# Performance work log

Hardware: AMD Instinct MI355X
Metric: run time of the kernel (lower is better)

Reference implementation:

```python
import jax, jax.numpy as jnp
import numpy as np

B, T, C = 4, 2048, 1024
H = 16
HD = C // H


def setup_inputs() -> dict:
    key = jax.random.key(0)
    k1, k2, k3 = jax.random.split(key, 3)
    x = jax.random.normal(k1, (B, T, C), dtype=jnp.float32)
    w_qkv = jax.random.normal(k2, (C, 3 * C), dtype=jnp.float32) * (C ** -0.5)
    w_proj = jax.random.normal(k3, (C, C), dtype=jnp.float32) * (C ** -0.5)
    b_proj = jnp.zeros((C,), dtype=jnp.float32)
    return {"x": x, "w_qkv": w_qkv, "w_proj": w_proj, "b_proj": b_proj}


def reference(x, w_qkv, w_proj, b_proj):
    Bd, Td, Cd = x.shape
    scale = HD ** -0.5
    qkv = x @ w_qkv  # [B,T,3C]
    q, k, v = jnp.split(qkv, 3, axis=-1)
    # [B,H,T,HD]
    q = q.reshape(Bd, Td, H, HD).transpose(0, 2, 1, 3)
    k = k.reshape(Bd, Td, H, HD).transpose(0, 2, 1, 3)
    v = v.reshape(Bd, Td, H, HD).transpose(0, 2, 1, 3)
    att = jnp.einsum('bhqd,bhkd->bhqk', q, k) * scale
    causal = jnp.triu(jnp.ones((Td, Td), dtype=bool), k=1)
    att = jnp.where(causal, -jnp.inf, att)
    att = jax.nn.softmax(att, axis=-1)
    y = jnp.einsum('bhqk,bhkd->bhqd', att, v)
    y = y.transpose(0, 2, 1, 3).reshape(Bd, Td, Cd)
    return y @ w_proj + b_proj
```

## Files before the change

kernel.cpp:

```cpp
#include <hip/hip_runtime.h>

typedef unsigned short u16;
typedef __attribute__((ext_vector_type(8))) short short8;
typedef __attribute__((ext_vector_type(4))) float floatx4;
typedef __attribute__((ext_vector_type(4))) unsigned short ushort4v;

#define B_ 4
#define T_ 2048
#define C_ 1024
#define H_ 16
#define HD_ 64

static __device__ __forceinline__ u16 f2bf(float f) {
  union { float f; unsigned int i; } c; c.f = f;
  unsigned int u = c.i;
  return (u16)((u + 0x7FFFu + ((u >> 16) & 1u)) >> 16);
}

static __device__ __forceinline__ void gload16(const u16* g, u16* l) {
  __builtin_amdgcn_global_load_lds(
      (const __attribute__((address_space(1))) unsigned int*)(g),
      (__attribute__((address_space(3))) unsigned int*)(l), 16, 0, 0);
}

__global__ __launch_bounds__(256) void prep_k(const float* __restrict__ x,
                                              const float* __restrict__ w_qkv,
                                              const float* __restrict__ w_proj,
                                              u16* __restrict__ xbf,
                                              u16* __restrict__ wqkvT,
                                              u16* __restrict__ wprojT) {
  const int bid = blockIdx.x;
  if (bid < 8192) {
    const int i = bid * 256 + threadIdx.x;
    const float4 f = ((const float4*)x)[i];
    ushort4v o;
    o.x = f2bf(f.x); o.y = f2bf(f.y); o.z = f2bf(f.z); o.w = f2bf(f.w);
    *(ushort4v*)(xbf + (size_t)i * 4) = o;
    return;
  }
  __shared__ u16 tile[32][33];
  const float* in;
  u16* out;
  int R, Cc, tb;
  if (bid < 11264) {
    in = w_qkv; out = wqkvT; R = C_; Cc = 3 * C_; tb = bid - 8192;
  } else {
    in = w_proj; out = wprojT; R = C_; Cc = C_; tb = bid - 11264;
  }
  const int tpr = Cc / 32;
  const int bx = (tb % tpr) * 32;
  const int by = (tb / tpr) * 32;
  const int tx = threadIdx.x & 31;
  const int ty = threadIdx.x >> 5;
  #pragma unroll
  for (int i = ty; i < 32; i += 8)
    tile[i][tx] = f2bf(in[(size_t)(by + i) * Cc + bx + tx]);
  __syncthreads();
  #pragma unroll
  for (int i = ty; i < 32; i += 8)
    out[(size_t)(bx + i) * R + by + tx] = tile[tx][i];
}

__global__ __launch_bounds__(256) void vtrans_k(const u16* __restrict__ qkv,
                                                u16* __restrict__ vt) {
  __shared__ u16 tile[64][74];
  const int tt = blockIdx.x;
  const int bh = blockIdx.y;
  const int b = bh >> 4, h = bh & 15;
  const int tid = threadIdx.x;
  const u16* src = qkv + ((size_t)b * T_ + tt * 64) * (3 * C_) + 2 * C_ + h * HD_;
  #pragma unroll
  for (int ss = tid; ss < 512; ss += 256) {
    const int row = ss >> 3, c8 = (ss & 7) * 8;
    *(short8*)(&tile[row][c8]) = *(const short8*)(src + (size_t)row * (3 * C_) + c8);
  }
  __syncthreads();
  u16* dst = vt + (size_t)bh * HD_ * T_ + tt * 64;
  #pragma unroll
  for (int ss = tid; ss < 512; ss += 256) {
    const int tc = (ss & 7) * 8, d = ss >> 3;
    short8 o;
    #pragma unroll
    for (int j = 0; j < 8; j++) o[j] = (short)tile[tc + j][d];
    *(short8*)(dst + (size_t)d * T_ + tc) = o;
  }
}

template <int MODE>
__global__ __launch_bounds__(256) void gemm_bt(const u16* __restrict__ A,
                                               const u16* __restrict__ Bt,
                                               u16* __restrict__ outb,
                                               float* __restrict__ outf,
                                               const float* __restrict__ bias,
                                               int M, int N, int K) {
  __shared__ __align__(16) u16 As[2][128 * 32];
  __shared__ __align__(16) u16 Bs[2][128 * 32];
  const int tN = blockIdx.x * 128;
  const int tM = blockIdx.y * 128;
  const int tid = threadIdx.x;
  const int wave = tid >> 6;
  const int lane = tid & 63;
  const int lr = lane & 15;
  const int quad = lane >> 4;
  const int wm = (wave >> 1) * 64;
  const int wn = (wave & 1) * 64;

  const int srow = lane >> 2;
  const int skofs = ((lane & 3) ^ ((lane >> 3) & 3)) * 8;

  const floatx4 zf = {0.f, 0.f, 0.f, 0.f};
  floatx4 acc[4][4];
  #pragma unroll
  for (int i = 0; i < 4; i++)
    #pragma unroll
    for (int j = 0; j < 4; j++) acc[i][j] = zf;

  const int csw = (lr >> 1) & 3;

  for (int k0 = 0; k0 < K; k0 += 64) {
    __syncthreads();
    #pragma unroll
    for (int half = 0; half < 2; half++) {
      const int kk = k0 + half * 32;
      #pragma unroll
      for (int j = 0; j < 2; j++) {
        const int seg = wave * 2 + j;
        const int row = seg * 16 + srow;
        gload16(A + (size_t)(tM + row) * K + kk + skofs, &As[half][seg * 512]);
        gload16(Bt + (size_t)(tN + row) * K + kk + skofs, &Bs[half][seg * 512]);
      }
    }
    __syncthreads();

    #pragma unroll
    for (int half = 0; half < 2; half++) {
      short8 af[4], bfr[4];
      #pragma unroll
      for (int mt = 0; mt < 4; mt++)
        af[mt] = *(const short8*)(&As[half][(wm + mt * 16 + lr) * 32 + ((quad ^ csw) * 8)]);
      #pragma unroll
      for (int nt = 0; nt < 4; nt++)
        bfr[nt] = *(const short8*)(&Bs[half][(wn + nt * 16 + lr) * 32 + ((quad ^ csw) * 8)]);
      #pragma unroll
      for (int mt = 0; mt < 4; mt++)
        #pragma unroll
        for (int nt = 0; nt < 4; nt++)
          acc[mt][nt] = __builtin_amdgcn_mfma_f32_16x16x32_bf16(af[mt], bfr[nt],
                                                                acc[mt][nt], 0, 0, 0);
    }
  }

  #pragma unroll
  for (int mt = 0; mt < 4; mt++) {
    const int m0 = tM + wm + mt * 16 + quad * 4;
    #pragma unroll
    for (int nt = 0; nt < 4; nt++) {
      const int n = tN + wn + nt * 16 + lr;
      #pragma unroll
      for (int r = 0; r < 4; r++) {
        const float v = acc[mt][nt][r];
        const size_t m = (size_t)(m0 + r);
        if (MODE == 2) outf[m * N + n] = v + bias[n];
        else           outb[m * N + n] = f2bf(v);
      }
    }
  }
}

__global__ __launch_bounds__(256, 4) void attn_k(const u16* __restrict__ qkv,
                                                 const u16* __restrict__ vt,
                                                 u16* __restrict__ y) {
  __shared__ __align__(16) u16 Ks[64 * 64];
  __shared__ __align__(16) u16 Vs[64 * 64];
  __shared__ __align__(16) u16 PsA[4][16 * 72];
  __shared__ __align__(16) u16 PsB[4][16 * 72];
  const int qp = blockIdx.x;
  const int bh = blockIdx.y;
  const int b = bh >> 4, h = bh & 15;
  const int tid = threadIdx.x;
  const int wave = tid >> 6;
  const int lane = tid & 63;
  const int lr = lane & 15;
  const int quad = lane >> 4;
  const int qtA = qp, qtB = 31 - qp;

  const int srow = lane >> 3;
  const int skofs = ((lane & 7) ^ ((lane >> 3) & 7)) * 8;
  const int gsw = lr & 7;

  const size_t RS = 3 * C_;
  const u16* qcol = qkv + (size_t)b * T_ * RS + h * HD_;
  const u16* kcol = qcol + C_;

  const size_t qrA = (size_t)(qtA * 64 + wave * 16 + lr) * RS;
  const size_t qrB = (size_t)(qtB * 64 + wave * 16 + lr) * RS;
  const short8 aq0A = *(const short8*)(qcol + qrA + quad * 8);
  const short8 aq1A = *(const short8*)(qcol + qrA + 32 + quad * 8);
  const short8 aq0B = *(const short8*)(qcol + qrB + quad * 8);
  const short8 aq1B = *(const short8*)(qcol + qrB + 32 + quad * 8);

  const floatx4 zf = {0.f, 0.f, 0.f, 0.f};
  const float C1 = 0.125f * 1.44269504f;
  const float C2 = -16.0f * 1.44269504f;

  floatx4 accA[4], accB[4];
  #pragma unroll
  for (int i = 0; i < 4; i++) { accA[i] = zf; accB[i] = zf; }
  float psumA[4] = {0.f, 0.f, 0.f, 0.f}, psumB[4] = {0.f, 0.f, 0.f, 0.f};

  for (int kt = 0; kt <= qtB; kt++) {
    const bool doA = (kt <= qtA);
    const bool diagA = (kt == qtA), diagB = (kt == qtB);
    __syncthreads();
    #pragma unroll
    for (int j = 0; j < 2; j++) {
      const int seg = wave * 2 + j;
      const int row = seg * 8 + srow;
      gload16(kcol + (size_t)(kt * 64 + row) * RS + skofs, &Ks[seg * 512]);
      gload16(vt + ((size_t)bh * HD_ + row) * T_ + kt * 64 + skofs, &Vs[seg * 512]);
    }
    __syncthreads();

    #pragma unroll
    for (int nt = 0; nt < 4; nt++) {
      const short8 bk0 =
          *(const short8*)(&Ks[(nt * 16 + lr) * 64 + ((quad ^ gsw) * 8)]);
      const short8 bk1 =
          *(const short8*)(&Ks[(nt * 16 + lr) * 64 + (((quad + 4) ^ gsw) * 8)]);
      {
        floatx4 s = __builtin_amdgcn_mfma_f32_16x16x32_bf16(
            aq1B, bk1,
            __builtin_amdgcn_mfma_f32_16x16x32_bf16(aq0B, bk0, zf, 0, 0, 0),
            0, 0, 0);
        #pragma unroll
        for (int r = 0; r < 4; r++) {
          float pe = __builtin_amdgcn_exp2f(fmaf(s[r], C1, C2));
          if (diagB && (nt * 16 + lr > wave * 16 + quad * 4 + r)) pe = 0.f;
          psumB[r] += pe;
          union { float f; unsigned int i; } cc; cc.f = pe;
          PsB[wave][(quad * 4 + r) * 72 + nt * 16 + lr] = (u16)(cc.i >> 16);
        }
      }
      if (doA) {
        floatx4 s = __builtin_amdgcn_mfma_f32_16x16x32_bf16(
            aq1A, bk1,
            __builtin_amdgcn_mfma_f32_16x16x32_bf16(aq0A, bk0, zf, 0, 0, 0),
            0, 0, 0);
        #pragma unroll
        for (int r = 0; r < 4; r++) {
          float pe = __builtin_amdgcn_exp2f(fmaf(s[r], C1, C2));
          if (diagA && (nt * 16 + lr > wave * 16 + quad * 4 + r)) pe = 0.f;
          psumA[r] += pe;
          union { float f; unsigned int i; } cc; cc.f = pe;
          PsA[wave][(quad * 4 + r) * 72 + nt * 16 + lr] = (u16)(cc.i >> 16);
        }
      }
    }
    const short8 apB0 = *(const short8*)(&PsB[wave][lr * 72 + quad * 8]);
    const short8 apB1 = *(const short8*)(&PsB[wave][lr * 72 + 32 + quad * 8]);
    short8 apA0, apA1;
    if (doA) {
      apA0 = *(const short8*)(&PsA[wave][lr * 72 + quad * 8]);
      apA1 = *(const short8*)(&PsA[wave][lr * 72 + 32 + quad * 8]);
    }
    #pragma unroll
    for (int dt = 0; dt < 4; dt++) {
      const short8 bv0 =
          *(const short8*)(&Vs[(dt * 16 + lr) * 64 + ((quad ^ gsw) * 8)]);
      const short8 bv1 =
          *(const short8*)(&Vs[(dt * 16 + lr) * 64 + (((quad + 4) ^ gsw) * 8)]);
      accB[dt] = __builtin_amdgcn_mfma_f32_16x16x32_bf16(apB0, bv0, accB[dt], 0, 0, 0);
      accB[dt] = __builtin_amdgcn_mfma_f32_16x16x32_bf16(apB1, bv1, accB[dt], 0, 0, 0);
      if (doA) {
        accA[dt] = __builtin_amdgcn_mfma_f32_16x16x32_bf16(apA0, bv0, accA[dt], 0, 0, 0);
        accA[dt] = __builtin_amdgcn_mfma_f32_16x16x32_bf16(apA1, bv1, accA[dt], 0, 0, 0);
      }
    }
  }

  #pragma unroll
  for (int ph = 0; ph < 2; ph++) {
    const int qt = ph ? qtB : qtA;
    const floatx4* acc = ph ? accB : accA;
    const float* ps = ph ? psumB : psumA;
    const int rowg0 = qt * 64 + wave * 16 + quad * 4;
    #pragma unroll
    for (int r = 0; r < 4; r++) {
      float s = ps[r];
      #pragma unroll
      for (int off = 1; off < 16; off <<= 1) s += __shfl_xor(s, off, 64);
      const float inv = 1.f / s;
      const int t = rowg0 + r;
      #pragma unroll
      for (int dt = 0; dt < 4; dt++) {
        const int d = dt * 16 + lr;
        y[((size_t)(b * T_ + t)) * C_ + h * HD_ + d] = f2bf(acc[dt][r] * inv);
      }
    }
  }
}

extern "C" void kernel_launch(void* const* d_in, const int* in_sizes, int n_in,
                              void* d_out, int out_size, void* d_ws, size_t ws_size,
                              hipStream_t stream) {
  const float* x      = (const float*)d_in[0];
  const float* w_qkv  = (const float*)d_in[1];
  const float* w_proj = (const float*)d_in[2];
  const float* b_proj = (const float*)d_in[3];
  float* out = (float*)d_out;

  u16* ws = (u16*)d_ws;
  const size_t SZ = (size_t)B_ * T_ * C_;
  u16* xbf    = ws;
  u16* wqkvT  = xbf + SZ;
  u16* wprojT = wqkvT + (size_t)3 * C_ * C_;
  u16* qkvw   = wprojT + (size_t)C_ * C_;
  u16* vtw    = qkvw + 3 * SZ;
  u16* yw     = xbf;

  prep_k<<<12288, 256, 0, stream>>>(x, w_qkv, w_proj, xbf, wqkvT, wprojT);
  gemm_bt<1><<<dim3(3 * C_ / 128, B_ * T_ / 128), 256, 0, stream>>>(
      xbf, wqkvT, qkvw, nullptr, nullptr, B_ * T_, 3 * C_, C_);
  vtrans_k<<<dim3(T_ / 64, B_ * H_), 256, 0, stream>>>(qkvw, vtw);
  attn_k<<<dim3(16, B_ * H_), 256, 0, stream>>>(qkvw, vtw, yw);
  gemm_bt<2><<<dim3(C_ / 128, B_ * T_ / 128), 256, 0, stream>>>(
      yw, wprojT, nullptr, out, b_proj, B_ * T_, C_, C_);
}
```

Measured before the change: 266.6 us.

## Compute transposed scores so P stays in registers, dropping LDS round-trip

The score MFMA now computes S^T (K as the A operand, Q as B), so each lane holds exp'd probabilities already laid out as the B operand of the PV MFMA. This removes the per-wave P shared-memory buffers and their writes and reads. V fragments are gathered with split 4-element LDS reads to match the new k-ordering. The output is written as vectorized 4-element stores, and the row-sum reduction shrinks to two shuffles. The grid is flattened to 1D with a remapped block index, presumably to change how blocks are scheduled across heads. The changes add register pressure and 8-byte LDS reads in place of 16-byte ones.

```diff
diff --git a/kernel.cpp b/kernel.cpp
--- a/kernel.cpp
+++ b/kernel.cpp
@@ -2,6 +2,7 @@
 
 typedef unsigned short u16;
 typedef __attribute__((ext_vector_type(8))) short short8;
+typedef __attribute__((ext_vector_type(4))) short short4v;
 typedef __attribute__((ext_vector_type(4))) float floatx4;
 typedef __attribute__((ext_vector_type(4))) unsigned short ushort4v;
 
@@ -15,6 +16,10 @@
   union { float f; unsigned int i; } c; c.f = f;
   unsigned int u = c.i;
   return (u16)((u + 0x7FFFu + ((u >> 16) & 1u)) >> 16);
+}
+static __device__ __forceinline__ u16 truncbf(float f) {
+  union { float f; unsigned int i; } c; c.f = f;
+  return (u16)(c.i >> 16);
 }
 
 static __device__ __forceinline__ void gload16(const u16* g, u16* l) {
@@ -172,10 +177,10 @@
                                                  u16* __restrict__ y) {
   __shared__ __align__(16) u16 Ks[64 * 64];
   __shared__ __align__(16) u16 Vs[64 * 64];
-  __shared__ __align__(16) u16 PsA[4][16 * 72];
-  __shared__ __align__(16) u16 PsB[4][16 * 72];
-  const int qp = blockIdx.x;
-  const int bh = blockIdx.y;
+  const int bid = blockIdx.x;
+  const int s = bid >> 3;
+  const int qp = s >> 3;
+  const int bh = ((s & 7) << 3) | (bid & 7);
   const int b = bh >> 4, h = bh & 15;
   const int tid = threadIdx.x;
   const int wave = tid >> 6;
@@ -206,7 +211,7 @@
   floatx4 accA[4], accB[4];
   #pragma unroll
   for (int i = 0; i < 4; i++) { accA[i] = zf; accB[i] = zf; }
-  float psumA[4] = {0.f, 0.f, 0.f, 0.f}, psumB[4] = {0.f, 0.f, 0.f, 0.f};
+  float psumA = 0.f, psumB = 0.f;
 
   for (int kt = 0; kt <= qtB; kt++) {
     const bool doA = (kt <= qtA);
@@ -221,6 +226,7 @@
     }
     __syncthreads();
 
+    float peA[4][4], peB[4][4];
     #pragma unroll
     for (int nt = 0; nt < 4; nt++) {
       const short8 bk0 =
@@ -228,52 +234,57 @@
       const short8 bk1 =
           *(const short8*)(&Ks[(nt * 16 + lr) * 64 + (((quad + 4) ^ gsw) * 8)]);
       {
-        floatx4 s = __builtin_amdgcn_mfma_f32_16x16x32_bf16(
-            aq1B, bk1,
-            __builtin_amdgcn_mfma_f32_16x16x32_bf16(aq0B, bk0, zf, 0, 0, 0),
+        floatx4 st = __builtin_amdgcn_mfma_f32_16x16x32_bf16(
+            bk1, aq1B,
+            __builtin_amdgcn_mfma_f32_16x16x32_bf16(bk0, aq0B, zf, 0, 0, 0),
             0, 0, 0);
         #pragma unroll
         for (int r = 0; r < 4; r++) {
-          float pe = __builtin_amdgcn_exp2f(fmaf(s[r], C1, C2));
-          if (diagB && (nt * 16 + lr > wave * 16 + quad * 4 + r)) pe = 0.f;
-          psumB[r] += pe;
-          union { float f; unsigned int i; } cc; cc.f = pe;
-          PsB[wave][(quad * 4 + r) * 72 + nt * 16 + lr] = (u16)(cc.i >> 16);
+          float pe = __builtin_amdgcn_exp2f(fmaf(st[r], C1, C2));
+          if (diagB && (nt * 16 + quad * 4 + r > wave * 16 + lr)) pe = 0.f;
+          peB[nt][r] = pe;
+          psumB += pe;
         }
       }
       if (doA) {
-        floatx4 s = __builtin_amdgcn_mfma_f32_16x16x32_bf16(
-            aq1A, bk1,
-            __builtin_amdgcn_mfma_f32_16x16x32_bf16(aq0A, bk0, zf, 0, 0, 0),
+        floatx4 st = __builtin_amdgcn_mfma_f32_16x16x32_bf16(
+            bk1, aq1A,
+            __builtin_amdgcn_mfma_f32_16x16x32_bf16(bk0, aq0A, zf, 0, 0, 0),
             0, 0, 0);
         #pragma unroll
         for (int r = 0; r < 4; r++) {
-          float pe = __builtin_amdgcn_exp2f(fmaf(s[r], C1, C2));
-          if (diagA && (nt * 16 + lr > wave * 16 + quad * 4 + r)) pe = 0.f;
-          psumA[r] += pe;
-          union { float f; unsigned int i; } cc; cc.f = pe;
-          PsA[wave][(quad * 4 + r) * 72 + nt * 16 + lr] = (u16)(cc.i >> 16);
+          float pe = __builtin_amdgcn_exp2f(fmaf(st[r], C1, C2));
+          if (diagA && (nt * 16 + quad * 4 + r > wave * 16 + lr)) pe = 0.f;
+          peA[nt][r] = pe;
+          psumA += pe;
         }
       }
     }
-    const short8 apB0 = *(const short8*)(&PsB[wave][lr * 72 + quad * 8]);
-    const short8 apB1 = *(const short8*)(&PsB[wave][lr * 72 + 32 + quad * 8]);
-    short8 apA0, apA1;
-    if (doA) {
-      apA0 = *(const short8*)(&PsA[wave][lr * 72 + quad * 8]);
-      apA1 = *(const short8*)(&PsA[wave][lr * 72 + 32 + quad * 8]);
-    }
-    #pragma unroll
-    for (int dt = 0; dt < 4; dt++) {
-      const short8 bv0 =
-          *(const short8*)(&Vs[(dt * 16 + lr) * 64 + ((quad ^ gsw) * 8)]);
-      const short8 bv1 =
-          *(const short8*)(&Vs[(dt * 16 + lr) * 64 + (((quad + 4) ^ gsw) * 8)]);
-      accB[dt] = __builtin_amdgcn_mfma_f32_16x16x32_bf16(apB0, bv0, accB[dt], 0, 0, 0);
-      accB[dt] = __builtin_amdgcn_mfma_f32_16x16x32_bf16(apB1, bv1, accB[dt], 0, 0, 0);
-      if (doA) {
-        accA[dt] = __builtin_amdgcn_mfma_f32_16x16x32_bf16(apA0, bv0, accA[dt], 0, 0, 0);
-        accA[dt] = __builtin_amdgcn_mfma_f32_16x16x32_bf16(apA1, bv1, accA[dt], 0, 0, 0);
+
+    short8 pB[2], pA[2];
+    #pragma unroll
+    for (int h2 = 0; h2 < 2; h2++) {
+      #pragma unroll
+      for (int j = 0; j < 8; j++) {
+        pB[h2][j] = (short)truncbf(peB[2 * h2 + (j >> 2)][j & 3]);
+        if (doA) pA[h2][j] = (short)truncbf(peA[2 * h2 + (j >> 2)][j & 3]);
+      }
+    }
+
+    #pragma unroll
+    for (int h2 = 0; h2 < 2; h2++) {
+      #pragma unroll
+      for (int dt = 0; dt < 4; dt++) {
+        const int base = (dt * 16 + lr) * 64;
+        const int cl = h2 * 4 + (quad >> 1);
+        const int off_lo = ((cl ^ gsw) * 8) + (quad & 1) * 4;
+        const int off_hi = (((cl + 2) ^ gsw) * 8) + (quad & 1) * 4;
+        const short4v vlo = *(const short4v*)(&Vs[base + off_lo]);
+        const short4v vhi = *(const short4v*)(&Vs[base + off_hi]);
+        const short8 av = __builtin_shufflevector(vlo, vhi, 0, 1, 2, 3, 4, 5, 6, 7);
+        accB[dt] = __builtin_amdgcn_mfma_f32_16x16x32_bf16(av, pB[h2], accB[dt], 0, 0, 0);
+        if (doA)
+          accA[dt] = __builtin_amdgcn_mfma_f32_16x16x32_bf16(av, pA[h2], accA[dt], 0, 0, 0);
       }
     }
   }
@@ -282,20 +293,18 @@
   for (int ph = 0; ph < 2; ph++) {
     const int qt = ph ? qtB : qtA;
     const floatx4* acc = ph ? accB : accA;
-    const float* ps = ph ? psumB : psumA;
-    const int rowg0 = qt * 64 + wave * 16 + quad * 4;
-    #pragma unroll
-    for (int r = 0; r < 4; r++) {
-      float s = ps[r];
-      #pragma unroll
-      for (int off = 1; off < 16; off <<= 1) s += __shfl_xor(s, off, 64);
-      const float inv = 1.f / s;
-      const int t = rowg0 + r;
-      #pragma unroll
-      for (int dt = 0; dt < 4; dt++) {
-        const int d = dt * 16 + lr;
-        y[((size_t)(b * T_ + t)) * C_ + h * HD_ + d] = f2bf(acc[dt][r] * inv);
-      }
+    float ssum = ph ? psumB : psumA;
+    ssum += __shfl_xor(ssum, 16, 64);
+    ssum += __shfl_xor(ssum, 32, 64);
+    const float inv = 1.f / ssum;
+    const int qg = qt * 64 + wave * 16 + lr;
+    u16* yrow = y + ((size_t)(b * T_ + qg)) * C_ + h * HD_;
+    #pragma unroll
+    for (int dt = 0; dt < 4; dt++) {
+      ushort4v o;
+      #pragma unroll
+      for (int r = 0; r < 4; r++) o[r] = f2bf(acc[dt][r] * inv);
+      *(ushort4v*)(yrow + dt * 16 + quad * 4) = o;
     }
   }
 }
@@ -322,7 +331,7 @@
   gemm_bt<1><<<dim3(3 * C_ / 128, B_ * T_ / 128), 256, 0, stream>>>(
       xbf, wqkvT, qkvw, nullptr, nullptr, B_ * T_, 3 * C_, C_);
   vtrans_k<<<dim3(T_ / 64, B_ * H_), 256, 0, stream>>>(qkvw, vtw);
-  attn_k<<<dim3(16, B_ * H_), 256, 0, stream>>>(qkvw, vtw, yw);
+  attn_k<<<1024, 256, 0, stream>>>(qkvw, vtw, yw);
   gemm_bt<2><<<dim3(C_ / 128, B_ * T_ / 128), 256, 0, stream>>>(
       yw, wprojT, nullptr, out, b_proj, B_ * T_, C_, C_);
 }
```

Result: faster. 244.3 us (-8.4%).
